# Performance work log

Measured on AMD Instinct MI355X. Metric: run time of the kernel, lower is better.

Reference implementation:

```python
import jax, jax.numpy as jnp
import numpy as np

# Module hyperparameters (init_kwargs)
HIDDEN_SIZE = 1024
BITS = 4                      # bits_per_route
NUM_ROUTES = HIDDEN_SIZE // BITS   # 256
ALPHABET = 1 << BITS               # 16 (alphabet_size = 2**bits_per_route)
MEM_DIM = 16
NGRAMS = (2, 3)
B, T = 2, 1024


def _quantize_codes(q_logits):
    """Hard-quantize route logits to integer codes in [0, ALPHABET).
    code[b,t,r] = sum_m (logit[b,t,r,m] > 0) << m  (sign-bit packing)."""
    Bsz, Tlen, _ = q_logits.shape
    bits = (q_logits.reshape(Bsz, Tlen, NUM_ROUTES, BITS) > 0).astype(jnp.int32)
    weights = jnp.int32(1) << jnp.arange(BITS, dtype=jnp.int32)  # [BITS]
    return jnp.sum(bits * weights, axis=-1)  # [B, T, R] int32


def _window_addr(codes, n):
    """Base-ALPHABET n-gram address for each window of n consecutive codes.
    addr[b,j,r] = sum_p codes[b, j+p, r] * ALPHABET**p,  j in [0, T-n]."""
    Bsz, Tlen, R = codes.shape
    V = Tlen - n + 1
    addr = jnp.zeros((Bsz, V, R), dtype=jnp.int32)
    for p in range(n):  # tiny fixed loop over ngram order
        addr = addr + codes[:, p:p + V, :] * (ALPHABET ** p)
    return addr


def setup_inputs() -> dict:
    key = jax.random.key(0)
    k1, k2, k3 = jax.random.split(key, 3)
    q_logits = jax.random.normal(k1, (B, T, HIDDEN_SIZE), dtype=jnp.float32)
    table_2 = jax.random.normal(k2, (NUM_ROUTES * ALPHABET ** 2, MEM_DIM), dtype=jnp.float32) * 0.02
    table_3 = jax.random.normal(k3, (NUM_ROUTES * ALPHABET ** 3, MEM_DIM), dtype=jnp.float32) * 0.02
    return {"q_logits": q_logits, "table_2": table_2, "table_3": table_3}


def reference(q_logits, table_2, table_3):
    """Forward of RouteExactNgramMemory: quantize logits to route codes,
    build bit-packed n-gram hash addresses, gather per-route memory vectors.
    Output: flat memory [B, T, num_ngram_orders * num_routes * mem_dim];
    the first n-1 timesteps of each n-gram branch are zero."""
    tables = (table_2, table_3)
    codes = _quantize_codes(q_logits)                      # [B,T,R]
    Bsz, Tlen = codes.shape[:2]
    route_off = jnp.arange(NUM_ROUTES, dtype=jnp.int32)
    outs = []
    for tbl, n in zip(tables, NGRAMS):
        addr = _window_addr(codes, n)                      # [B,V,R]
        gidx = addr + (route_off * (ALPHABET ** n))[None, None, :]
        vals = tbl[gidx]                                   # [B,V,R,D] gather
        outs.append(jnp.pad(vals, ((0, 0), (n - 1, 0), (0, 0), (0, 0))))
    mem = jnp.stack(outs, axis=2)                          # [B,T,O,R,D]
    return mem.reshape(Bsz, Tlen, -1)
```

## Files before the change

kernel.cpp:

```cpp
#include <hip/hip_runtime.h>


#define BB 2
#define TT 1024
#define RR 256
#define DD 16

using f4 = __attribute__((ext_vector_type(4))) float;

__global__ void codes_kernel(const float* __restrict__ q,
                             unsigned char* __restrict__ codes) {
    int tid = blockIdx.x * blockDim.x + threadIdx.x;
    f4 v = reinterpret_cast<const f4*>(q)[tid];
    unsigned char c = (v.x > 0.0f ? 1u : 0u)
                    | (v.y > 0.0f ? 2u : 0u)
                    | (v.z > 0.0f ? 4u : 0u)
                    | (v.w > 0.0f ? 8u : 0u);
    codes[tid] = c;
}

__global__ void gather_kernel(const unsigned char* __restrict__ codes,
                              const float* __restrict__ t2,
                              const float* __restrict__ t3,
                              float* __restrict__ out) {
    int bid  = blockIdx.x;
    int rgrp = bid & 7;
    int tch  = (bid >> 3) & 127;
    int b    = bid >> 10;
    int tx   = threadIdx.x;
    int part = tx & 3;
    int rlo  = (tx >> 2) & 31;
    int tlo  = tx >> 7;
    int r    = (rgrp << 5) + rlo;
    int t0   = (tch << 1) + tlo;

    const unsigned char* cb = codes + b * (TT * RR) + r;
    const f4* t2v = reinterpret_cast<const f4*>(t2);
    const f4* t3v = reinterpret_cast<const f4*>(t3);
    f4* ov = reinterpret_cast<f4*>(out);
    f4 z = {0.f, 0.f, 0.f, 0.f};

    int c0[4], c1[4], c2[4];
#pragma unroll
    for (int k = 0; k < 4; ++k) {
        int t = t0 + k * 256;
        c0[k] = cb[t * RR];
        c1[k] = (t >= 1) ? cb[(t - 1) * RR] : 0;
        c2[k] = (t >= 2) ? cb[(t - 2) * RR] : 0;
    }

    f4 v2[4], v3[4];
#pragma unroll
    for (int k = 0; k < 4; ++k) {
        int t = t0 + k * 256;
        v2[k] = (t >= 1)
            ? t2v[(((r << 8) + c1[k] + (c0[k] << 4)) << 2) + part] : z;
        v3[k] = (t >= 2)
            ? t3v[(((r << 12) + c2[k] + (c1[k] << 4) + (c0[k] << 8)) << 2) + part] : z;
    }

#pragma unroll
    for (int k = 0; k < 4; ++k) {
        int t = t0 + k * 256;
        size_t base = (((size_t)(b * TT + t) * 2) * RR + r) * 4 + part;
        __builtin_nontemporal_store(v2[k], ov + base);
        __builtin_nontemporal_store(v3[k], ov + base + RR * 4);
    }
}

extern "C" void kernel_launch(void* const* d_in, const int* in_sizes, int n_in,
                              void* d_out, int out_size, void* d_ws, size_t ws_size,
                              hipStream_t stream) {
    const float* q  = (const float*)d_in[0];
    const float* t2 = (const float*)d_in[1];
    const float* t3 = (const float*)d_in[2];
    float* out = (float*)d_out;
    unsigned char* codes = (unsigned char*)d_ws;

    codes_kernel<<<(BB * TT * RR) / 256, 256, 0, stream>>>(q, codes);

    gather_kernel<<<2048, 256, 0, stream>>>(codes, t2, t3, out);
}
```

Measured before the change: 28.25 us.

## Fuse code quantization into gather kernel using shared-memory code tile

Merges the quantization and gather kernels into one launch. Each block quantizes the q_logits it needs (8 timesteps plus a 2-step halo, 32 routes) into a shared-memory code tile, then runs the table gathers from there. Timesteps per block become contiguous instead of strided. This removes a kernel launch and the workspace round-trip for codes, at the cost of re-reading halo rows of q and adding a block barrier.

```diff
diff --git a/kernel.cpp b/kernel.cpp
--- a/kernel.cpp
+++ b/kernel.cpp
@@ -4,64 +4,74 @@
 #define BB 2
 #define TT 1024
 #define RR 256
-#define DD 16
 
 using f4 = __attribute__((ext_vector_type(4))) float;
 
-__global__ void codes_kernel(const float* __restrict__ q,
-                             unsigned char* __restrict__ codes) {
-    int tid = blockIdx.x * blockDim.x + threadIdx.x;
-    f4 v = reinterpret_cast<const f4*>(q)[tid];
-    unsigned char c = (v.x > 0.0f ? 1u : 0u)
-                    | (v.y > 0.0f ? 2u : 0u)
-                    | (v.z > 0.0f ? 4u : 0u)
-                    | (v.w > 0.0f ? 8u : 0u);
-    codes[tid] = c;
-}
+__global__ __launch_bounds__(256) void fused_kernel(
+    const float* __restrict__ q,
+    const float* __restrict__ t2,
+    const float* __restrict__ t3,
+    float* __restrict__ out) {
+    int bid   = blockIdx.x;
+    int rgrp  = bid & 7;
+    int tch   = (bid >> 3) & 127;
+    int b     = bid >> 10;
+    int t0    = tch << 3;
+    int rbase = rgrp << 5;
 
-__global__ void gather_kernel(const unsigned char* __restrict__ codes,
-                              const float* __restrict__ t2,
-                              const float* __restrict__ t3,
-                              float* __restrict__ out) {
-    int bid  = blockIdx.x;
-    int rgrp = bid & 7;
-    int tch  = (bid >> 3) & 127;
-    int b    = bid >> 10;
-    int tx   = threadIdx.x;
+    __shared__ unsigned char lcode[10 * 32];
+
+    int tx = threadIdx.x;
+
+    const f4* qv = reinterpret_cast<const f4*>(q);
+#pragma unroll
+    for (int i = 0; i < 2; ++i) {
+        int item = tx + (i << 8);
+        if (item < 320) {
+            int ti  = item >> 5;
+            int rlo = item & 31;
+            int t   = t0 - 2 + ti;
+            unsigned char code = 0;
+            if (t >= 0) {
+                f4 v = qv[(size_t)(b * TT + t) * RR + rbase + rlo];
+                code = (v.x > 0.0f ? 1u : 0u)
+                     | (v.y > 0.0f ? 2u : 0u)
+                     | (v.z > 0.0f ? 4u : 0u)
+                     | (v.w > 0.0f ? 8u : 0u);
+            }
+            lcode[ti * 32 + rlo] = code;
+        }
+    }
+    __syncthreads();
+
     int part = tx & 3;
     int rlo  = (tx >> 2) & 31;
     int tlo  = tx >> 7;
-    int r    = (rgrp << 5) + rlo;
-    int t0   = (tch << 1) + tlo;
+    int r    = rbase + rlo;
 
-    const unsigned char* cb = codes + b * (TT * RR) + r;
+    unsigned char cc[6];
+#pragma unroll
+    for (int j = 0; j < 6; ++j)
+        cc[j] = lcode[(tlo * 4 + j) * 32 + rlo];
+
     const f4* t2v = reinterpret_cast<const f4*>(t2);
     const f4* t3v = reinterpret_cast<const f4*>(t3);
-    f4* ov = reinterpret_cast<f4*>(out);
     f4 z = {0.f, 0.f, 0.f, 0.f};
-
-    int c0[4], c1[4], c2[4];
-#pragma unroll
-    for (int k = 0; k < 4; ++k) {
-        int t = t0 + k * 256;
-        c0[k] = cb[t * RR];
-        c1[k] = (t >= 1) ? cb[(t - 1) * RR] : 0;
-        c2[k] = (t >= 2) ? cb[(t - 2) * RR] : 0;
-    }
-
     f4 v2[4], v3[4];
 #pragma unroll
     for (int k = 0; k < 4; ++k) {
-        int t = t0 + k * 256;
+        int t  = t0 + tlo * 4 + k;
+        int a2 = cc[k], a1 = cc[k + 1], a0 = cc[k + 2];
         v2[k] = (t >= 1)
-            ? t2v[(((r << 8) + c1[k] + (c0[k] << 4)) << 2) + part] : z;
+            ? t2v[(((r << 8) + a1 + (a0 << 4)) << 2) + part] : z;
         v3[k] = (t >= 2)
-            ? t3v[(((r << 12) + c2[k] + (c1[k] << 4) + (c0[k] << 8)) << 2) + part] : z;
+            ? t3v[(((r << 12) + a2 + (a1 << 4) + (a0 << 8)) << 2) + part] : z;
     }
 
+    f4* ov = reinterpret_cast<f4*>(out);
 #pragma unroll
     for (int k = 0; k < 4; ++k) {
-        int t = t0 + k * 256;
+        int t = t0 + tlo * 4 + k;
         size_t base = (((size_t)(b * TT + t) * 2) * RR + r) * 4 + part;
         __builtin_nontemporal_store(v2[k], ov + base);
         __builtin_nontemporal_store(v3[k], ov + base + RR * 4);
@@ -75,9 +85,6 @@
     const float* t2 = (const float*)d_in[1];
     const float* t3 = (const float*)d_in[2];
     float* out = (float*)d_out;
-    unsigned char* codes = (unsigned char*)d_ws;
 
-    codes_kernel<<<(BB * TT * RR) / 256, 256, 0, stream>>>(q, codes);
-
-    gather_kernel<<<2048, 256, 0, stream>>>(codes, t2, t3, out);
+    fused_kernel<<<2048, 256, 0, stream>>>(q, t2, t3, out);
 }
```

Result: faster. 23.99 us, median of 2 (-15.1%).
